# Kernel tuning notes

Hardware: AMD Instinct MI355X
Metric: run time of the kernel (lower is better)

The kernel has to match this reference:

```python
import jax, jax.numpy as jnp
import numpy as np

# Module hyper-parameters (match init_kwargs)
H = 8          # num_heads
F = 32         # attention_filters
HF = H * F     # 256, equals input channels C
RY, RX = 2, 2  # spatial_radius
PH, PW = 2 * RY + 1, 2 * RX + 1
S = PH * PW    # 25 neighbor offsets


def setup_inputs() -> dict:
    key = jax.random.key(0)
    ks = jax.random.split(key, 6)
    B, Y, X, C = 8, 128, 128, 256
    x = jax.random.normal(ks[0], (B, Y, X, C), dtype=jnp.float32)
    sc = 0.02
    Wq = jax.random.normal(ks[1], (C, HF), dtype=jnp.float32) * sc
    Wk = jax.random.normal(ks[2], (C, HF), dtype=jnp.float32) * sc
    Wv = jax.random.normal(ks[3], (C, HF), dtype=jnp.float32) * sc
    Wout = jax.random.normal(ks[4], (HF, C), dtype=jnp.float32) * sc
    pos_emb = jax.random.normal(ks[5], (S, HF), dtype=jnp.float32) * sc
    return {"x": x, "Wq": Wq, "Wk": Wk, "Wv": Wv, "Wout": Wout, "pos_emb": pos_emb}


def _centers(n, r):
    # clipped patch-center coordinate for each position
    c = jnp.arange(n)
    return jnp.clip(c, r, n - r - 1)


def reference(x, Wq, Wk, Wv, Wout, pos_emb):
    B, Y, X, C = x.shape
    dtype = x.dtype
    # 1x1 conv projections == channel matmuls
    Q = jnp.einsum('byxc,cf->byxf', x, Wq)
    K = jnp.einsum('byxc,cf->byxf', x, Wk)
    V = jnp.einsum('byxc,cf->byxf', x, Wv)

    # query spatial positional embedding (relative position to clipped center)
    yc = _centers(Y, RY)
    xc = _centers(X, RX)
    y_rel = jnp.arange(Y) - yc + RY          # [Y]
    x_rel = jnp.arange(X) - xc + RX          # [X]
    q_idx = y_rel[:, None] * PW + x_rel[None, :]  # [Y, X]
    Q = Q + pos_emb[q_idx]                   # [B,Y,X,HF]
    Q = Q.reshape(B, Y, X, H, F)

    scale = jnp.asarray(1.0 / np.sqrt(F), dtype)

    offsets = [(dy, dx) for dy in range(-RY, RY + 1) for dx in range(-RX, RX + 1)]

    # pass 1: per-offset scores (loop over fixed 25-neighborhood, rest vectorized)
    scores = []
    for s_idx, (dy, dx) in enumerate(offsets):
        ny = jnp.clip(yc + dy, 0, Y - 1)     # [Y]
        nx = jnp.clip(xc + dx, 0, X - 1)     # [X]
        Kn = K[:, ny][:, :, nx] + pos_emb[s_idx]        # [B,Y,X,HF]
        Kn = Kn.reshape(B, Y, X, H, F)
        scores.append(jnp.einsum('byxhf,byxhf->byxh', Q, Kn) * scale)
    scores = jnp.stack(scores, axis=-1)      # [B,Y,X,H,S]
    weights = jax.nn.softmax(scores, axis=-1)

    # pass 2: weighted value accumulation
    out_acc = jnp.zeros((B, Y, X, H, F), dtype=dtype)
    for s_idx, (dy, dx) in enumerate(offsets):
        ny = jnp.clip(yc + dy, 0, Y - 1)
        nx = jnp.clip(xc + dx, 0, X - 1)
        Vn = V[:, ny][:, :, nx].reshape(B, Y, X, H, F)
        out_acc = out_acc + weights[..., s_idx, None] * Vn

    out_acc = out_acc.reshape(B, Y, X, HF)
    out = jnp.einsum('byxf,fc->byxc', out_acc, Wout)
    return out
```

## Files before the change

### kernel.cpp

```cpp
#include <hip/hip_runtime.h>

#define DEVI __device__ __forceinline__

typedef short v8s __attribute__((ext_vector_type(8)));
typedef float v4f __attribute__((ext_vector_type(4)));
typedef unsigned short u16;

typedef __attribute__((address_space(3))) unsigned int lds_u32;
typedef const __attribute__((address_space(1))) unsigned int glb_u32;

DEVI float bf2f(short s) {
  union { unsigned u; float f; } cv;
  cv.u = ((unsigned)(u16)s) << 16;
  return cv.f;
}
DEVI short f2bf(float f) {
  union { float f; unsigned u; } cv; cv.f = f;
  unsigned u = cv.u;
  return (short)((u + 0x7FFFu + ((u >> 16) & 1u)) >> 16);
}
DEVI void gld16(const void* g, void* l) {
  __builtin_amdgcn_global_load_lds((glb_u32*)g, (lds_u32*)l, 16, 0, 0);
}

__global__ void prep_weights(const float* __restrict__ Wq, const float* __restrict__ Wk,
                             const float* __restrict__ Wv, const float* __restrict__ Wout,
                             short* __restrict__ WcT, short* __restrict__ WoT) {
  int n = blockIdx.x;
  int k = threadIdx.x;
  float v;
  if (n < 256)      v = Wq[k * 256 + n];
  else if (n < 512) v = Wk[k * 256 + (n - 256)];
  else              v = Wv[k * 256 + (n - 512)];
  WcT[n * 256 + k] = f2bf(v);
  if (n < 256) WoT[n * 256 + k] = f2bf(Wout[k * 256 + n]);
}

__global__ void x_cast(const float* __restrict__ x, short* __restrict__ xb) {
  for (size_t gidx = (size_t)blockIdx.x * 256 + threadIdx.x; gidx < 4194304;
       gidx += (size_t)4096 * 256) {
    const float4* src = reinterpret_cast<const float4*>(x + gidx * 8);
    float4 a = src[0], c = src[1];
    v8s pk;
    pk[0] = f2bf(a.x); pk[1] = f2bf(a.y); pk[2] = f2bf(a.z); pk[3] = f2bf(a.w);
    pk[4] = f2bf(c.x); pk[5] = f2bf(c.y); pk[6] = f2bf(c.z); pk[7] = f2bf(c.w);
    *reinterpret_cast<v8s*>(xb + gidx * 8) = pk;
  }
}

__launch_bounds__(256, 3)
__global__ void proj_gemm(const short* __restrict__ xb, const short* __restrict__ WcT,
                          const float* __restrict__ pos_emb,
                          short* __restrict__ Qb, short* __restrict__ Kb,
                          short* __restrict__ Vb) {
  __shared__ short As[128 * 64];
  __shared__ short Bs[128 * 64];
  const int t = threadIdx.x;
  const int bi = blockIdx.x;
  const int xcd = bi & 7;
  const int j = bi >> 3;
  const int mgl = j / 6, nt = j % 6;
  const int mtg = xcd * 32 + mgl;
  const int m0 = mtg * 512;
  const int n0 = nt * 128;
  const int wave = t >> 6, lane = t & 63;
  const int wm = (wave & 1) * 64, wn = (wave >> 1) * 64;
  const int lr = lane & 15, g = lane >> 4;

  const int ro = lane >> 3;
  const int colb = ((lane & 7) * 16) ^ (ro << 4);
  const char* aSrc0 = reinterpret_cast<const char*>(xb + (size_t)(m0 + ro) * 256) + colb;
  const char* bSrc  = reinterpret_cast<const char*>(WcT + (size_t)(n0 + ro) * 256) + colb;

#pragma unroll 1
  for (int u = 0; u < 4; ++u) {
    const char* aSrc = aSrc0 + (size_t)u * 128 * 512;

    v4f acc[4][4];
#pragma unroll
    for (int i = 0; i < 4; ++i)
#pragma unroll
      for (int jj = 0; jj < 4; ++jj) acc[i][jj] = (v4f){0.f, 0.f, 0.f, 0.f};

#pragma unroll 1
    for (int ks = 0; ks < 4; ++ks) {
      __syncthreads();
#pragma unroll
      for (int c = 0; c < 4; ++c) {
        int cc = wave * 4 + c;
        gld16(aSrc + (size_t)cc * 8 * 512 + ks * 128, (char*)As + cc * 1024);
        gld16(bSrc + (size_t)cc * 8 * 512 + ks * 128, (char*)Bs + cc * 1024);
      }
      __syncthreads();
#pragma unroll
      for (int kk = 0; kk < 2; ++kk) {
        v8s af[4], bfr[4];
#pragma unroll
        for (int i = 0; i < 4; ++i) {
          int row = wm + i * 16 + lr;
          int byte = (row * 128 + kk * 64 + g * 16) ^ ((row & 7) << 4);
          af[i] = *reinterpret_cast<const v8s*>(reinterpret_cast<const char*>(As) + byte);
        }
#pragma unroll
        for (int jj = 0; jj < 4; ++jj) {
          int rn = wn + jj * 16 + lr;
          int byte = (rn * 128 + kk * 64 + g * 16) ^ ((rn & 7) << 4);
          bfr[jj] = *reinterpret_cast<const v8s*>(reinterpret_cast<const char*>(Bs) + byte);
        }
#pragma unroll
        for (int i = 0; i < 4; ++i)
#pragma unroll
          for (int jj = 0; jj < 4; ++jj)
            acc[i][jj] = __builtin_amdgcn_mfma_f32_16x16x32_bf16(af[i], bfr[jj], acc[i][jj], 0, 0, 0);
      }
    }

#pragma unroll
    for (int i = 0; i < 4; ++i) {
#pragma unroll
      for (int jj = 0; jj < 4; ++jj) {
        int colg = n0 + wn + jj * 16 + lr;
#pragma unroll
        for (int r = 0; r < 4; ++r) {
          int p = m0 + u * 128 + wm + i * 16 + g * 4 + r;
          float v = acc[i][jj][r];
          if (nt < 2) {
            int yy = (p >> 7) & 127, xx = p & 127;
            int qi = (yy - min(max(yy, 2), 125) + 2) * 5 + (xx - min(max(xx, 2), 125) + 2);
            v += pos_emb[qi * 256 + colg];
            Qb[(size_t)p * 256 + colg] = f2bf(v);
          } else if (nt < 4) {
            Kb[(size_t)p * 256 + (colg - 256)] = f2bf(v);
          } else {
            Vb[(size_t)p * 256 + (colg - 512)] = f2bf(v);
          }
        }
      }
    }
  }
}

__launch_bounds__(256, 4)
__global__ void attn_kernel(const short* __restrict__ Qb, const short* __restrict__ Kb,
                            const short* __restrict__ Vb, const float* __restrict__ pos_emb,
                            short* __restrict__ ACC) {
  __shared__ float pe[25 * 256];
  for (int i = threadIdx.x; i < 1600; i += 256) {
    float4 vv = reinterpret_cast<const float4*>(pos_emb)[i];
    int w = i * 4;
    int f = w & 255;
    int dst = (w & ~255) + (f ^ ((f >> 5) << 2));
    *reinterpret_cast<float4*>(pe + dst) = vv;
  }

  const int t = threadIdx.x;
  const int half = t & 1, h = (t >> 1) & 7, pl = t >> 4;
  const int id = blockIdx.x;
  const int b = id & 7;
  const int local = id >> 3;
  const int bx = local & 31, by = local >> 5;
  const int xx = bx * 4 + (pl & 3);
  const int yy = by * 4 + (pl >> 2);
  const int yc = min(max(yy, 2), 125), xc = min(max(xx, 2), 125);
  const int fo = h * 32 + half * 16;
  const int hx4 = h << 2;
  const size_t pbase = ((size_t)((b * 128 + yy) * 128 + xx)) * 256 + fo;
  const size_t cbase = ((size_t)((b * 128 + yc) * 128 + xc)) * 256 + fo;
  const float SCALE = 0.17677669529663689f;

  float q[16];
  {
    v8s q0 = *reinterpret_cast<const v8s*>(Qb + pbase);
    v8s q1 = *reinterpret_cast<const v8s*>(Qb + pbase + 8);
#pragma unroll
    for (int e = 0; e < 8; ++e) { q[e] = bf2f(q0[e]); q[8 + e] = bf2f(q1[e]); }
  }
  __syncthreads();

  float l = 0.f;
  float oa[16];
#pragma unroll
  for (int f = 0; f < 16; ++f) oa[f] = 0.f;

  const short* kb = Kb + cbase;
  const short* vb = Vb + cbase;
  const float* pb = pe + h * 32;
  const int j0 = (half * 16) ^ hx4;
  const int j1 = (half * 16 + 4) ^ hx4;
  const int j2 = (half * 16 + 8) ^ hx4;
  const int j3 = (half * 16 + 12) ^ hx4;

#pragma unroll 1
  for (int dy = -2; dy <= 2; ++dy) {
    const short* krow = kb + dy * (128 * 256);
    const short* vrow = vb + dy * (128 * 256);
    const float* prow = pb + ((dy + 2) * 5) * 256;
#pragma unroll 1
    for (int dx = -2; dx <= 2; ++dx) {
      const short* kp = krow + dx * 256;
      const short* vp = vrow + dx * 256;
      const float* pp = prow + (dx + 2) * 256;
      v8s k0 = *reinterpret_cast<const v8s*>(kp);
      v8s k1 = *reinterpret_cast<const v8s*>(kp + 8);
      v8s v0 = *reinterpret_cast<const v8s*>(vp);
      v8s v1 = *reinterpret_cast<const v8s*>(vp + 8);
      float4 p0 = *reinterpret_cast<const float4*>(pp + j0);
      float4 p1 = *reinterpret_cast<const float4*>(pp + j1);
      float4 p2 = *reinterpret_cast<const float4*>(pp + j2);
      float4 p3 = *reinterpret_cast<const float4*>(pp + j3);
      float d0 = 0.f, d1 = 0.f, d2 = 0.f, d3 = 0.f;
#pragma unroll
      for (int e = 0; e < 4; ++e) {
        d0 = fmaf(q[e], bf2f(k0[e]), d0);
        d1 = fmaf(q[4 + e], bf2f(k0[4 + e]), d1);
        d2 = fmaf(q[8 + e], bf2f(k1[e]), d2);
        d3 = fmaf(q[12 + e], bf2f(k1[4 + e]), d3);
      }
      d0 = fmaf(q[0], p0.x, d0); d0 = fmaf(q[1], p0.y, d0);
      d0 = fmaf(q[2], p0.z, d0); d0 = fmaf(q[3], p0.w, d0);
      d1 = fmaf(q[4], p1.x, d1); d1 = fmaf(q[5], p1.y, d1);
      d1 = fmaf(q[6], p1.z, d1); d1 = fmaf(q[7], p1.w, d1);
      d2 = fmaf(q[8], p2.x, d2); d2 = fmaf(q[9], p2.y, d2);
      d2 = fmaf(q[10], p2.z, d2); d2 = fmaf(q[11], p2.w, d2);
      d3 = fmaf(q[12], p3.x, d3); d3 = fmaf(q[13], p3.y, d3);
      d3 = fmaf(q[14], p3.z, d3); d3 = fmaf(q[15], p3.w, d3);
      float part = ((d0 + d1) + (d2 + d3)) * SCALE;
      float full = part + __shfl_xor(part, 1);
      float w = __expf(full);
      l += w;
#pragma unroll
      for (int e = 0; e < 8; ++e) oa[e] = fmaf(w, bf2f(v0[e]), oa[e]);
#pragma unroll
      for (int e = 0; e < 8; ++e) oa[8 + e] = fmaf(w, bf2f(v1[e]), oa[8 + e]);
    }
  }

  float inv = 1.f / l;
  v8s o0, o1;
#pragma unroll
  for (int e = 0; e < 8; ++e) { o0[e] = f2bf(oa[e] * inv); o1[e] = f2bf(oa[8 + e] * inv); }
  *reinterpret_cast<v8s*>(ACC + pbase) = o0;
  *reinterpret_cast<v8s*>(ACC + pbase + 8) = o1;
}

__launch_bounds__(256, 3)
__global__ void out_gemm(const short* __restrict__ A, const short* __restrict__ WoT,
                         float* __restrict__ out) {
  __shared__ short As[128 * 64];
  __shared__ short Bs[128 * 64];
  const int t = threadIdx.x;
  const int bi = blockIdx.x;
  const int xcd = bi & 7;
  const int j = bi >> 3;
  const int mgl = j / 2, nt = j % 2;
  const int mtg = xcd * 64 + mgl;
  const int m0 = mtg * 256;
  const int n0 = nt * 128;
  const int wave = t >> 6, lane = t & 63;
  const int wm = (wave & 1) * 64, wn = (wave >> 1) * 64;
  const int lr = lane & 15, g = lane >> 4;

  const int ro = lane >> 3;
  const int colb = ((lane & 7) * 16) ^ (ro << 4);
  const char* aSrc0 = reinterpret_cast<const char*>(A + (size_t)(m0 + ro) * 256) + colb;
  const char* bSrc  = reinterpret_cast<const char*>(WoT + (size_t)(n0 + ro) * 256) + colb;

#pragma unroll 1
  for (int u = 0; u < 2; ++u) {
    const char* aSrc = aSrc0 + (size_t)u * 128 * 512;

    v4f acc[4][4];
#pragma unroll
    for (int i = 0; i < 4; ++i)
#pragma unroll
      for (int jj = 0; jj < 4; ++jj) acc[i][jj] = (v4f){0.f, 0.f, 0.f, 0.f};

#pragma unroll 1
    for (int ks = 0; ks < 4; ++ks) {
      __syncthreads();
#pragma unroll
      for (int c = 0; c < 4; ++c) {
        int cc = wave * 4 + c;
        gld16(aSrc + (size_t)cc * 8 * 512 + ks * 128, (char*)As + cc * 1024);
        gld16(bSrc + (size_t)cc * 8 * 512 + ks * 128, (char*)Bs + cc * 1024);
      }
      __syncthreads();
#pragma unroll
      for (int kk = 0; kk < 2; ++kk) {
        v8s af[4], bfr[4];
#pragma unroll
        for (int i = 0; i < 4; ++i) {
          int row = wm + i * 16 + lr;
          int byte = (row * 128 + kk * 64 + g * 16) ^ ((row & 7) << 4);
          af[i] = *reinterpret_cast<const v8s*>(reinterpret_cast<const char*>(As) + byte);
        }
#pragma unroll
        for (int jj = 0; jj < 4; ++jj) {
          int rn = wn + jj * 16 + lr;
          int byte = (rn * 128 + kk * 64 + g * 16) ^ ((rn & 7) << 4);
          bfr[jj] = *reinterpret_cast<const v8s*>(reinterpret_cast<const char*>(Bs) + byte);
        }
#pragma unroll
        for (int i = 0; i < 4; ++i)
#pragma unroll
          for (int jj = 0; jj < 4; ++jj)
            acc[i][jj] = __builtin_amdgcn_mfma_f32_16x16x32_bf16(af[i], bfr[jj], acc[i][jj], 0, 0, 0);
      }
    }

#pragma unroll
    for (int i = 0; i < 4; ++i) {
#pragma unroll
      for (int jj = 0; jj < 4; ++jj) {
        int colg = n0 + wn + jj * 16 + lr;
#pragma unroll
        for (int r = 0; r < 4; ++r) {
          int p = m0 + u * 128 + wm + i * 16 + g * 4 + r;
          out[(size_t)p * 256 + colg] = acc[i][jj][r];
        }
      }
    }
  }
}

extern "C" void kernel_launch(void* const* d_in, const int* in_sizes, int n_in,
                              void* d_out, int out_size, void* d_ws, size_t ws_size,
                              hipStream_t stream) {
  const float* x       = (const float*)d_in[0];
  const float* Wq      = (const float*)d_in[1];
  const float* Wk      = (const float*)d_in[2];
  const float* Wv      = (const float*)d_in[3];
  const float* Wout    = (const float*)d_in[4];
  const float* pos_emb = (const float*)d_in[5];
  float* out = (float*)d_out;

  char* ws = (char*)d_ws;
  short* WcT  = (short*)ws;
  short* WoT  = (short*)(ws + 393216);
  short* Qb   = (short*)(ws + 524288);
  short* Kb   = Qb + (size_t)131072 * 256;
  short* Vb   = Kb + (size_t)131072 * 256;
  short* ACCb = Vb + (size_t)131072 * 256;
  short* xb   = ACCb;

  prep_weights<<<768, 256, 0, stream>>>(Wq, Wk, Wv, Wout, WcT, WoT);
  x_cast<<<4096, 256, 0, stream>>>(x, xb);
  proj_gemm<<<1536, 256, 0, stream>>>(xb, WcT, pos_emb, Qb, Kb, Vb);
  attn_kernel<<<8192, 256, 0, stream>>>(Qb, Kb, Vb, pos_emb, ACCb);
  out_gemm<<<1024, 256, 0, stream>>>(ACCb, WoT, out);
}
```

Baseline: 377.5 us.

## Double-buffer A tiles and keep B resident in projection GEMM; prefetch K/V in attention

The projection GEMM now loads the full 128x256 weight tile into LDS once and double-buffers the activation tiles, so the next A tile is fetched while MFMAs run on the current one. The four M sub-tiles become one 16-step pipelined loop with a single barrier per step. Launch bounds drop from 3 to 1 blocks per SIMD because LDS use grows to 96KB, which lowers occupancy. Separately, the attention loop software-prefetches the next neighbor's K/V vectors into registers so the global load latency of one offset overlaps the compute of the previous one.

```diff
diff --git a/kernel.cpp b/kernel.cpp
--- a/kernel.cpp
+++ b/kernel.cpp
@@ -22,6 +22,8 @@
 DEVI void gld16(const void* g, void* l) {
   __builtin_amdgcn_global_load_lds((glb_u32*)g, (lds_u32*)l, 16, 0, 0);
 }
+#define SBAR() __builtin_amdgcn_s_barrier()
+#define SCHED0() __builtin_amdgcn_sched_barrier(0)
 
 __global__ void prep_weights(const float* __restrict__ Wq, const float* __restrict__ Wk,
                              const float* __restrict__ Wv, const float* __restrict__ Wout,
@@ -48,13 +50,13 @@
   }
 }
 
-__launch_bounds__(256, 3)
+__launch_bounds__(256, 1)
 __global__ void proj_gemm(const short* __restrict__ xb, const short* __restrict__ WcT,
                           const float* __restrict__ pos_emb,
                           short* __restrict__ Qb, short* __restrict__ Kb,
                           short* __restrict__ Vb) {
-  __shared__ short As[128 * 64];
-  __shared__ short Bs[128 * 64];
+  __shared__ short Bs[4][128 * 64];
+  __shared__ short Aa[2][128 * 64];
   const int t = threadIdx.x;
   const int bi = blockIdx.x;
   const int xcd = bi & 7;
@@ -70,69 +72,91 @@
   const int ro = lane >> 3;
   const int colb = ((lane & 7) * 16) ^ (ro << 4);
   const char* aSrc0 = reinterpret_cast<const char*>(xb + (size_t)(m0 + ro) * 256) + colb;
-  const char* bSrc  = reinterpret_cast<const char*>(WcT + (size_t)(n0 + ro) * 256) + colb;
-
-#pragma unroll 1
-  for (int u = 0; u < 4; ++u) {
-    const char* aSrc = aSrc0 + (size_t)u * 128 * 512;
-
-    v4f acc[4][4];
-#pragma unroll
-    for (int i = 0; i < 4; ++i)
-#pragma unroll
-      for (int jj = 0; jj < 4; ++jj) acc[i][jj] = (v4f){0.f, 0.f, 0.f, 0.f};
-
-#pragma unroll 1
-    for (int ks = 0; ks < 4; ++ks) {
-      __syncthreads();
+  const char* bSrc0 = reinterpret_cast<const char*>(WcT + (size_t)(n0 + ro) * 256) + colb;
+
+#pragma unroll
+  for (int ks = 0; ks < 4; ++ks) {
+#pragma unroll
+    for (int c = 0; c < 4; ++c) {
+      int cc = wave * 4 + c;
+      gld16(bSrc0 + (size_t)cc * 8 * 512 + ks * 128, (char*)Bs[ks] + cc * 1024);
+    }
+  }
+#pragma unroll
+  for (int c = 0; c < 4; ++c) {
+    int cc = wave * 4 + c;
+    gld16(aSrc0 + (size_t)cc * 8 * 512, (char*)Aa[0] + cc * 1024);
+  }
+
+  v4f acc[4][4];
+#pragma unroll
+  for (int i = 0; i < 4; ++i)
+#pragma unroll
+    for (int jj = 0; jj < 4; ++jj) acc[i][jj] = (v4f){0.f, 0.f, 0.f, 0.f};
+
+#pragma unroll 1
+  for (int s = 0; s < 16; ++s) {
+    const int buf = s & 1;
+    asm volatile("s_waitcnt vmcnt(0)" ::: "memory");
+    SBAR();
+    SCHED0();
+
+    if (s < 15) {
+      const int sn = s + 1;
+      const char* aS = aSrc0 + (size_t)(sn >> 2) * 128 * 512 + (sn & 3) * 128;
 #pragma unroll
       for (int c = 0; c < 4; ++c) {
         int cc = wave * 4 + c;
-        gld16(aSrc + (size_t)cc * 8 * 512 + ks * 128, (char*)As + cc * 1024);
-        gld16(bSrc + (size_t)cc * 8 * 512 + ks * 128, (char*)Bs + cc * 1024);
-      }
-      __syncthreads();
-#pragma unroll
-      for (int kk = 0; kk < 2; ++kk) {
-        v8s af[4], bfr[4];
-#pragma unroll
-        for (int i = 0; i < 4; ++i) {
-          int row = wm + i * 16 + lr;
-          int byte = (row * 128 + kk * 64 + g * 16) ^ ((row & 7) << 4);
-          af[i] = *reinterpret_cast<const v8s*>(reinterpret_cast<const char*>(As) + byte);
-        }
+        gld16(aS + (size_t)cc * 8 * 512, (char*)Aa[buf ^ 1] + cc * 1024);
+      }
+    }
+
+    const char* aB = (const char*)Aa[buf];
+    const char* bB = (const char*)Bs[s & 3];
+#pragma unroll
+    for (int kk = 0; kk < 2; ++kk) {
+      v8s af[4], bfr[4];
+#pragma unroll
+      for (int i = 0; i < 4; ++i) {
+        int row = wm + i * 16 + lr;
+        int byte = (row * 128 + kk * 64 + g * 16) ^ ((row & 7) << 4);
+        af[i] = *reinterpret_cast<const v8s*>(aB + byte);
+      }
+#pragma unroll
+      for (int jj = 0; jj < 4; ++jj) {
+        int rn = wn + jj * 16 + lr;
+        int byte = (rn * 128 + kk * 64 + g * 16) ^ ((rn & 7) << 4);
+        bfr[jj] = *reinterpret_cast<const v8s*>(bB + byte);
+      }
+#pragma unroll
+      for (int i = 0; i < 4; ++i)
+#pragma unroll
+        for (int jj = 0; jj < 4; ++jj)
+          acc[i][jj] = __builtin_amdgcn_mfma_f32_16x16x32_bf16(af[i], bfr[jj], acc[i][jj], 0, 0, 0);
+    }
+
+    if ((s & 3) == 3) {
+      const int u = s >> 2;
+#pragma unroll
+      for (int i = 0; i < 4; ++i) {
 #pragma unroll
         for (int jj = 0; jj < 4; ++jj) {
-          int rn = wn + jj * 16 + lr;
-          int byte = (rn * 128 + kk * 64 + g * 16) ^ ((rn & 7) << 4);
-          bfr[jj] = *reinterpret_cast<const v8s*>(reinterpret_cast<const char*>(Bs) + byte);
-        }
-#pragma unroll
-        for (int i = 0; i < 4; ++i)
-#pragma unroll
-          for (int jj = 0; jj < 4; ++jj)
-            acc[i][jj] = __builtin_amdgcn_mfma_f32_16x16x32_bf16(af[i], bfr[jj], acc[i][jj], 0, 0, 0);
-      }
-    }
-
-#pragma unroll
-    for (int i = 0; i < 4; ++i) {
-#pragma unroll
-      for (int jj = 0; jj < 4; ++jj) {
-        int colg = n0 + wn + jj * 16 + lr;
-#pragma unroll
-        for (int r = 0; r < 4; ++r) {
-          int p = m0 + u * 128 + wm + i * 16 + g * 4 + r;
-          float v = acc[i][jj][r];
-          if (nt < 2) {
-            int yy = (p >> 7) & 127, xx = p & 127;
-            int qi = (yy - min(max(yy, 2), 125) + 2) * 5 + (xx - min(max(xx, 2), 125) + 2);
-            v += pos_emb[qi * 256 + colg];
-            Qb[(size_t)p * 256 + colg] = f2bf(v);
-          } else if (nt < 4) {
-            Kb[(size_t)p * 256 + (colg - 256)] = f2bf(v);
-          } else {
-            Vb[(size_t)p * 256 + (colg - 512)] = f2bf(v);
+          int colg = n0 + wn + jj * 16 + lr;
+#pragma unroll
+          for (int r = 0; r < 4; ++r) {
+            int p = m0 + u * 128 + wm + i * 16 + g * 4 + r;
+            float v = acc[i][jj][r];
+            if (nt < 2) {
+              int yy = (p >> 7) & 127, xx = p & 127;
+              int qi = (yy - min(max(yy, 2), 125) + 2) * 5 + (xx - min(max(xx, 2), 125) + 2);
+              v += pos_emb[qi * 256 + colg];
+              Qb[(size_t)p * 256 + colg] = f2bf(v);
+            } else if (nt < 4) {
+              Kb[(size_t)p * 256 + (colg - 256)] = f2bf(v);
+            } else {
+              Vb[(size_t)p * 256 + (colg - 512)] = f2bf(v);
+            }
+            acc[i][jj][r] = 0.f;
           }
         }
       }
@@ -190,20 +214,33 @@
   const int j2 = (half * 16 + 8) ^ hx4;
   const int j3 = (half * 16 + 12) ^ hx4;
 
+  v8s kn0, kn1, vn0, vn1;
+  {
+    const short* kp = kb + (-2 * 128 - 2) * 256;
+    const short* vp = vb + (-2 * 128 - 2) * 256;
+    kn0 = *reinterpret_cast<const v8s*>(kp);
+    kn1 = *reinterpret_cast<const v8s*>(kp + 8);
+    vn0 = *reinterpret_cast<const v8s*>(vp);
+    vn1 = *reinterpret_cast<const v8s*>(vp + 8);
+  }
+
 #pragma unroll 1
   for (int dy = -2; dy <= 2; ++dy) {
-    const short* krow = kb + dy * (128 * 256);
-    const short* vrow = vb + dy * (128 * 256);
     const float* prow = pb + ((dy + 2) * 5) * 256;
 #pragma unroll 1
     for (int dx = -2; dx <= 2; ++dx) {
-      const short* kp = krow + dx * 256;
-      const short* vp = vrow + dx * 256;
+      v8s k0 = kn0, k1 = kn1, v0 = vn0, v1 = vn1;
+      int ndx = dx + 1, ndy = dy;
+      if (ndx > 2) { ndx = -2; ndy = dy + 1; }
+      if (ndy <= 2) {
+        const short* kp2 = kb + (ndy * 128 + ndx) * 256;
+        const short* vp2 = vb + (ndy * 128 + ndx) * 256;
+        kn0 = *reinterpret_cast<const v8s*>(kp2);
+        kn1 = *reinterpret_cast<const v8s*>(kp2 + 8);
+        vn0 = *reinterpret_cast<const v8s*>(vp2);
+        vn1 = *reinterpret_cast<const v8s*>(vp2 + 8);
+      }
       const float* pp = prow + (dx + 2) * 256;
-      v8s k0 = *reinterpret_cast<const v8s*>(kp);
-      v8s k1 = *reinterpret_cast<const v8s*>(kp + 8);
-      v8s v0 = *reinterpret_cast<const v8s*>(vp);
-      v8s v1 = *reinterpret_cast<const v8s*>(vp + 8);
       float4 p0 = *reinterpret_cast<const float4*>(pp + j0);
       float4 p1 = *reinterpret_cast<const float4*>(pp + j1);
       float4 p2 = *reinterpret_cast<const float4*>(pp + j2);
```

Result: slower. 503.1 us (+33.3%).
